# Optimization experiments

Hardware: AMD Instinct MI355X
Metric: run time of the kernel (lower is better)

The kernel has to match this reference:

```python
import jax, jax.numpy as jnp
import numpy as np

B, T, L, C = 64, 1024, 68, 2
H = 256  # hidden size per direction
D_IN = L * C  # 136


def setup_inputs() -> dict:
    key = jax.random.key(0)
    ks = jax.random.split(key, 8)
    s_ih = 0.05
    s_hh = 1.0 / np.sqrt(H)
    return {
        "x": jax.random.normal(ks[0], (B, T, L, C), dtype=jnp.float32),
        "w_ih_f": jax.random.normal(ks[1], (4 * H, D_IN), dtype=jnp.float32) * s_ih,
        "w_hh_f": jax.random.normal(ks[2], (4 * H, H), dtype=jnp.float32) * s_hh,
        "b_ih_f": jnp.zeros((4 * H,), jnp.float32),
        "b_hh_f": jnp.zeros((4 * H,), jnp.float32),
        "w_ih_b": jax.random.normal(ks[3], (4 * H, D_IN), dtype=jnp.float32) * s_ih,
        "w_hh_b": jax.random.normal(ks[4], (4 * H, H), dtype=jnp.float32) * s_hh,
        "b_ih_b": jnp.zeros((4 * H,), jnp.float32),
        "b_hh_b": jnp.zeros((4 * H,), jnp.float32),
        "fc_w": jax.random.normal(ks[5], (5, 2 * H), dtype=jnp.float32) * 0.06,
        "fc_b": jnp.zeros((5,), jnp.float32),
    }


def _lstm_scan(x_proj, w_hh, b_hh):
    """x_proj: (T, B, 4H) precomputed input projections. Returns hidden seq (T, B, H).
    PyTorch gate order: i, f, g, o."""
    h_dim = w_hh.shape[1]
    bsz = x_proj.shape[1]

    def step(carry, gx):
        h, c = carry
        g = gx + h @ w_hh.T + b_hh  # (B, 4H)
        i, f, gg, o = jnp.split(g, 4, axis=-1)
        i = jax.nn.sigmoid(i)
        f = jax.nn.sigmoid(f)
        gg = jnp.tanh(gg)
        o = jax.nn.sigmoid(o)
        c = f * c + i * gg
        h = o * jnp.tanh(c)
        return (h, c), h

    h0 = jnp.zeros((bsz, h_dim), x_proj.dtype)
    _, hs = jax.lax.scan(step, (h0, h0), x_proj)
    return hs


def reference(x, w_ih_f, w_hh_f, b_ih_f, b_hh_f, w_ih_b, w_hh_b, b_ih_b, b_hh_b, fc_w, fc_b):
    bsz, t = x.shape[0], x.shape[1]
    xf = x.reshape(bsz, t, -1)            # (B, T, 136)
    xt = jnp.transpose(xf, (1, 0, 2))     # (T, B, 136) time-major for scan
    # Precompute input-to-hidden projections for both directions (big GEMM, outside scan).
    proj_f = xt @ w_ih_f.T + b_ih_f       # (T, B, 4H)
    proj_b = xt[::-1] @ w_ih_b.T + b_ih_b # reversed time for backward direction
    hs_f = _lstm_scan(proj_f, w_hh_f, b_hh_f)           # (T, B, H)
    hs_b = _lstm_scan(proj_b, w_hh_b, b_hh_b)[::-1]     # flip back to forward time
    out = jnp.concatenate([hs_f, hs_b], axis=-1)        # (T, B, 2H)
    out = jnp.transpose(out, (1, 0, 2))                 # (B, T, 2H)
    # Dropout is identity in eval mode.
    return out @ fc_w.T + fc_b                          # (B, T, 5)
```

## Files before the change

kernel.cpp:

```cpp
#include <hip/hip_runtime.h>
#include <hip/hip_bf16.h>
#include <stdint.h>

#define B_    64
#define T_    1024
#define DIN   136
#define DINP  160
#define H_    256
#define G4H   1024

typedef __bf16 bf16;
typedef __bf16 bf16x8 __attribute__((ext_vector_type(8)));
typedef float  floatx4 __attribute__((ext_vector_type(4)));
typedef int    int4v  __attribute__((ext_vector_type(4)));

__global__ void k_pack_x(const float* __restrict__ x, bf16* __restrict__ xp) {
  const int n = T_ * B_ * DINP;
  for (int i = blockIdx.x * blockDim.x + threadIdx.x; i < n; i += gridDim.x * blockDim.x) {
    int k  = i % DINP;
    int tb = i / DINP;
    int b  = tb % B_;
    int t  = tb / B_;
    float v = 0.f;
    if (k < DIN) v = x[(b * T_ + t) * DIN + k];
    xp[i] = (bf16)v;
  }
}

__global__ void k_pack_whh(const float* __restrict__ wf, const float* __restrict__ wb,
                           bf16* __restrict__ wp) {
  const int n = 2 * G4H * H_;
  for (int i = blockIdx.x * blockDim.x + threadIdx.x; i < n; i += gridDim.x * blockDim.x) {
    int k   = i & (H_ - 1);
    int r   = (i >> 8) & (G4H - 1);
    int dir = i >> 18;
    int orig = ((r & 3) << 8) | (r >> 2);
    const float* w = dir ? wb : wf;
    wp[i] = (bf16)w[orig * H_ + k];
  }
}

__global__ void k_pack_wih(const float* __restrict__ wf, const float* __restrict__ wb,
                           bf16* __restrict__ wp) {
  const int n = 2 * G4H * DINP;
  for (int i = blockIdx.x * blockDim.x + threadIdx.x; i < n; i += gridDim.x * blockDim.x) {
    int k   = i % DINP;
    int r   = (i / DINP) & (G4H - 1);
    int dir = i / (G4H * DINP);
    int orig = ((r & 3) << 8) | (r >> 2);
    const float* w = dir ? wb : wf;
    float v = (k < DIN) ? w[orig * DIN + k] : 0.f;
    wp[i] = (bf16)v;
  }
}

__global__ void k_pack_bias(const float* __restrict__ bihf, const float* __restrict__ bhhf,
                            const float* __restrict__ bihb, const float* __restrict__ bhhb,
                            float* __restrict__ bs) {
  int i = blockIdx.x * blockDim.x + threadIdx.x;
  if (i >= 2 * G4H) return;
  int r = i & (G4H - 1); int dir = i >> 10;
  int orig = ((r & 3) << 8) | (r >> 2);
  bs[i] = dir ? (bihb[orig] + bhhb[orig]) : (bihf[orig] + bhhf[orig]);
}

__global__ __launch_bounds__(256, 1) void k_lstm(
    const bf16* __restrict__ xp, const bf16* __restrict__ whhp,
    const bf16* __restrict__ wihp, const float* __restrict__ bs,
    bf16* __restrict__ hbuf, unsigned* __restrict__ cnt)
{
  __shared__ bf16 h_sm[2 * 16 * 264];
  unsigned short* h_su = (unsigned short*)h_sm;

  const int tid = threadIdx.x;
  const int w   = tid >> 6;
  const int l   = tid & 63;
  const int q   = l >> 4;
  const int m   = l & 15;

  const int wgid  = blockIdx.x;
  const int g     = wgid >> 2;
  const int qtr   = wgid & 3;
  const int dir   = g >> 2;
  const int btile = g & 3;
  const int rowbase = qtr * 256 + w * 64;

  bf16x8 wf[4][8];
  bf16x8 wif[4][5];
  floatx4 bias[4];
#pragma unroll
  for (int tl = 0; tl < 4; ++tl) {
    const bf16* wr = whhp + (size_t)(dir * G4H + rowbase + tl * 16 + m) * H_ + q * 8;
#pragma unroll
    for (int s = 0; s < 8; ++s) {
      int kk = (qtr * 2 + s) & 7;
      wf[tl][s] = *(const bf16x8*)(wr + kk * 32);
    }
    const bf16* wr2 = wihp + (size_t)(dir * G4H + rowbase + tl * 16 + m) * DINP + q * 8;
#pragma unroll
    for (int kk = 0; kk < 5; ++kk) wif[tl][kk] = *(const bf16x8*)(wr2 + kk * 32);
    bias[tl] = *(const floatx4*)(bs + dir * G4H + rowbase + tl * 16 + q * 4);
  }

  unsigned* const cptr    = cnt + g * T_;
  unsigned* const hbuf_dw = (unsigned*)hbuf;
  const size_t hb_g = (size_t)g * T_;

  float cst[4] = {0.f, 0.f, 0.f, 0.f};

  bf16x8 xf[5];
  {
    const int xt0 = dir ? (T_ - 1) : 0;
    const bf16* xr = xp + (size_t)(xt0 * B_ + btile * 16 + m) * DINP + q * 8;
#pragma unroll
    for (int kk = 0; kk < 5; ++kk) xf[kk] = *(const bf16x8*)(xr + kk * 32);
  }

  for (int t = 0; t < T_; ++t) {
    const int xt = dir ? (T_ - 1 - t) : t;
    floatx4 acc[4] = {bias[0], bias[1], bias[2], bias[3]};

#pragma unroll
    for (int kk = 0; kk < 5; ++kk) {
#pragma unroll
      for (int tl = 0; tl < 4; ++tl)
        acc[tl] = __builtin_amdgcn_mfma_f32_16x16x32_bf16(wif[tl][kk], xf[kk], acc[tl], 0, 0, 0);
    }
    if (t + 1 < T_) {
      const int xtn = dir ? (T_ - 2 - t) : (t + 1);
      const bf16* xr = xp + (size_t)(xtn * B_ + btile * 16 + m) * DINP + q * 8;
#pragma unroll
      for (int kk = 0; kk < 5; ++kk) xf[kk] = *(const bf16x8*)(xr + kk * 32);
    }

    if (t > 0) {
      const int p = (t - 1) & 1;
      const bf16* hrow = &h_sm[(p * 16 + m) * 264 + q * 8];

#pragma unroll
      for (int s = 0; s < 2; ++s) {
        int kk = (qtr * 2 + s) & 7;
        bf16x8 bfr = *(const bf16x8*)(hrow + kk * 32);
#pragma unroll
        for (int tl = 0; tl < 4; ++tl)
          acc[tl] = __builtin_amdgcn_mfma_f32_16x16x32_bf16(wf[tl][s], bfr, acc[tl], 0, 0, 0);
      }

      {
        unsigned v;
        for (;;) {
          unsigned lv = 0;
          if (l == 0) lv = __hip_atomic_load(cptr + (t - 1), __ATOMIC_RELAXED, __HIP_MEMORY_SCOPE_AGENT);
          v = (unsigned)__shfl((int)lv, 0);
          if (v >= 16u) break;
          __builtin_amdgcn_s_sleep(1);
        }
      }
      __atomic_signal_fence(__ATOMIC_SEQ_CST);

      {
        const int xtp = dir ? (xt + 1) : (xt - 1);
        const size_t base_dw = (hb_g + xtp) * 16 * 128;
        const int mm = tid >> 4, jj = tid & 15;
        unsigned svals[6];
#pragma unroll
        for (int pp = 0; pp < 3; ++pp) {
          int qq = (qtr + 1 + pp) & 3;
          const unsigned* sp = hbuf_dw + base_dw + (size_t)mm * 128 + qq * 32 + jj;
          svals[pp * 2 + 0] = __hip_atomic_load(sp,      __ATOMIC_RELAXED, __HIP_MEMORY_SCOPE_AGENT);
          svals[pp * 2 + 1] = __hip_atomic_load(sp + 16, __ATOMIC_RELAXED, __HIP_MEMORY_SCOPE_AGENT);
        }
#pragma unroll
        for (int pp = 0; pp < 3; ++pp) {
          int qq = (qtr + 1 + pp) & 3;
          unsigned* dst = (unsigned*)&h_su[(p * 16 + mm) * 264 + qq * 64];
          dst[jj]      = svals[pp * 2 + 0];
          dst[jj + 16] = svals[pp * 2 + 1];
        }
      }
      __syncthreads();

#pragma unroll
      for (int s = 2; s < 8; ++s) {
        int kk = (qtr * 2 + s) & 7;
        bf16x8 bfr = *(const bf16x8*)(hrow + kk * 32);
#pragma unroll
        for (int tl = 0; tl < 4; ++tl)
          acc[tl] = __builtin_amdgcn_mfma_f32_16x16x32_bf16(wf[tl][s], bfr, acc[tl], 0, 0, 0);
      }
    }

    unsigned short hu[4];
#pragma unroll
    for (int tl = 0; tl < 4; ++tl) {
      float pi = acc[tl][0], pf = acc[tl][1], pg = acc[tl][2], po = acc[tl][3];
      float ig = 1.f / (1.f + __expf(-pi));
      float fg = 1.f / (1.f + __expf(-pf));
      float og = 1.f / (1.f + __expf(-po));
      float gcl = fminf(fmaxf(pg, -15.f), 15.f);
      float e2  = __expf(2.f * gcl);
      float gg  = (e2 - 1.f) / (e2 + 1.f);
      float c   = fg * cst[tl] + ig * gg;
      cst[tl]   = c;
      float ccl = fminf(fmaxf(c, -15.f), 15.f);
      float ec  = __expf(2.f * ccl);
      float hv  = og * ((ec - 1.f) / (ec + 1.f));
      bf16 hb = (bf16)hv;
      hu[tl] = __builtin_bit_cast(unsigned short, hb);
    }

    {
      const size_t obase = ((hb_g + xt) * 16 + m) * 128 + (size_t)(qtr * 32 + w * 8);
#pragma unroll
      for (int tl = 0; tl < 4; ++tl) {
        int ov = __shfl_xor((int)(unsigned)hu[tl], 16);
        if ((q & 1) == 0) {
          unsigned dw = (unsigned)hu[tl] | ((unsigned)ov << 16);
          __hip_atomic_store(hbuf_dw + obase + tl * 2 + (q >> 1), dw,
                             __ATOMIC_RELAXED, __HIP_MEMORY_SCOPE_AGENT);
        }
      }
    }

    {
      const int pcur = t & 1;
      const int hidl = qtr * 64 + w * 16 + q;
#pragma unroll
      for (int tl = 0; tl < 4; ++tl)
        h_su[(pcur * 16 + m) * 264 + hidl + tl * 4] = hu[tl];
    }

    asm volatile("s_waitcnt vmcnt(0)" ::: "memory");
    __atomic_signal_fence(__ATOMIC_SEQ_CST);
    if (l == 0)
      __hip_atomic_fetch_add(cptr + t, 1u, __ATOMIC_RELAXED, __HIP_MEMORY_SCOPE_AGENT);
    __syncthreads();
  }
}

__global__ __launch_bounds__(512) void k_fc(const bf16* __restrict__ hbuf,
                                            const float* __restrict__ fcw,
                                            const float* __restrict__ fcb,
                                            float* __restrict__ out)
{
  __shared__ float wsm[5 * 512];
  __shared__ unsigned short hl[64 * 258];
  const int tid = threadIdx.x;
  const int t   = blockIdx.x;
  for (int i = tid; i < 2560; i += 512) wsm[i] = fcw[i];
  const int o = tid / 64, b = tid & 63;
  float acc = 0.f;
  for (int dirc = 0; dirc < 2; ++dirc) {
    __syncthreads();
    for (int i = tid; i < 8192; i += 512) {
      int bb = i >> 7, dd = i & 127;
      int gg = dirc * 4 + (bb >> 4), mm = bb & 15;
      ((unsigned*)hl)[bb * 129 + dd] =
          ((const unsigned*)hbuf)[((size_t)(gg * T_ + t) * 16 + mm) * 128 + dd];
    }
    __syncthreads();
    if (tid < 320) {
      const float* wr = &wsm[o * 512 + dirc * 256];
      const unsigned short* hr = &hl[b * 258];
      float a = 0.f;
#pragma unroll 8
      for (int h = 0; h < 256; ++h) {
        unsigned u = ((unsigned)hr[h]) << 16;
        a += wr[h] * __builtin_bit_cast(float, u);
      }
      acc += a;
    }
  }
  if (tid < 320) out[((size_t)b * T_ + t) * 5 + o] = acc + fcb[o];
}

extern "C" void kernel_launch(void* const* d_in, const int* in_sizes, int n_in,
                              void* d_out, int out_size, void* d_ws, size_t ws_size,
                              hipStream_t stream) {
  const float* x    = (const float*)d_in[0];
  const float* wihf = (const float*)d_in[1];
  const float* whhf = (const float*)d_in[2];
  const float* bihf = (const float*)d_in[3];
  const float* bhhf = (const float*)d_in[4];
  const float* wihb = (const float*)d_in[5];
  const float* whhb = (const float*)d_in[6];
  const float* bihb = (const float*)d_in[7];
  const float* bhhb = (const float*)d_in[8];
  const float* fcw  = (const float*)d_in[9];
  const float* fcb  = (const float*)d_in[10];
  float* out = (float*)d_out;

  char* ws = (char*)d_ws;
  bf16*     xp   = (bf16*)(ws + 0);
  bf16*     whhp = (bf16*)(ws + 20971520);
  bf16*     wihp = (bf16*)(ws + 22020096);
  float*    bsum = (float*)(ws + 22675456);
  unsigned* cnt  = (unsigned*)(ws + 22683648);
  bf16*     hseq = (bf16*)(ws + 22716416);
  (void)in_sizes; (void)n_in; (void)out_size; (void)ws_size;

  hipMemsetAsync(cnt, 0, 8 * T_ * sizeof(unsigned), stream);
  k_pack_x   <<<4096, 256, 0, stream>>>(x, xp);
  k_pack_whh <<<1024, 256, 0, stream>>>(whhf, whhb, whhp);
  k_pack_wih <<<640,  256, 0, stream>>>(wihf, wihb, wihp);
  k_pack_bias<<<8,    256, 0, stream>>>(bihf, bhhf, bihb, bhhb, bsum);
  k_lstm     <<<32,   256, 0, stream>>>(xp, whhp, wihp, bsum, hseq, cnt);
  k_fc       <<<1024, 512, 0, stream>>>(hseq, fcw, fcb, out);
}
```

Before: 3.091 ms.

## Rewrite LSTM with int8 recurrent MFMA, single-block-per-group, segmented precomputed projections

Replaces the bf16 recurrent GEMM with int8 MFMA. Weights are quantized per tile, and h is split into hi and lo int8 parts to keep precision. Each batch tile now runs in one 1024-thread block, removing the cross-workgroup atomic flag sync. The input projection moves out of the recurrence into a separate fp16 GEMM kernel, run in four time segments that alternate with the LSTM and FC kernels, with state carried through global memory. Fast exp2/rcp activations are used. The extra kernel launches and the reduced-precision recurrence risk accuracy and add overhead.

```diff
diff --git a/kernel.cpp b/kernel.cpp
--- a/kernel.cpp
+++ b/kernel.cpp
@@ -8,36 +8,22 @@
 #define DINP  160
 #define H_    256
 #define G4H   1024
+#define SEG   256
+#define NSEG  4
 
 typedef __bf16 bf16;
+typedef _Float16 f16;
 typedef __bf16 bf16x8 __attribute__((ext_vector_type(8)));
 typedef float  floatx4 __attribute__((ext_vector_type(4)));
 typedef int    int4v  __attribute__((ext_vector_type(4)));
-
-__global__ void k_pack_x(const float* __restrict__ x, bf16* __restrict__ xp) {
-  const int n = T_ * B_ * DINP;
-  for (int i = blockIdx.x * blockDim.x + threadIdx.x; i < n; i += gridDim.x * blockDim.x) {
-    int k  = i % DINP;
-    int tb = i / DINP;
-    int b  = tb % B_;
-    int t  = tb / B_;
-    float v = 0.f;
-    if (k < DIN) v = x[(b * T_ + t) * DIN + k];
-    xp[i] = (bf16)v;
-  }
-}
-
-__global__ void k_pack_whh(const float* __restrict__ wf, const float* __restrict__ wb,
-                           bf16* __restrict__ wp) {
-  const int n = 2 * G4H * H_;
-  for (int i = blockIdx.x * blockDim.x + threadIdx.x; i < n; i += gridDim.x * blockDim.x) {
-    int k   = i & (H_ - 1);
-    int r   = (i >> 8) & (G4H - 1);
-    int dir = i >> 18;
-    int orig = ((r & 3) << 8) | (r >> 2);
-    const float* w = dir ? wb : wf;
-    wp[i] = (bf16)w[orig * H_ + k];
-  }
+typedef _Float16 half4 __attribute__((ext_vector_type(4)));
+
+__device__ __forceinline__ float fsigm(float x) {
+  return __builtin_amdgcn_rcpf(1.f + __builtin_amdgcn_exp2f(x * -1.4426950408889634f));
+}
+__device__ __forceinline__ float ftanh(float x) {
+  float e = __builtin_amdgcn_exp2f(x * 2.8853900817779268f);
+  return 1.f - 2.f * __builtin_amdgcn_rcpf(e + 1.f);
 }
 
 __global__ void k_pack_wih(const float* __restrict__ wf, const float* __restrict__ wb,
@@ -64,199 +50,244 @@
   bs[i] = dir ? (bihb[orig] + bhhb[orig]) : (bihf[orig] + bhhf[orig]);
 }
 
-__global__ __launch_bounds__(256, 1) void k_lstm(
-    const bf16* __restrict__ xp, const bf16* __restrict__ whhp,
-    const bf16* __restrict__ wihp, const float* __restrict__ bs,
-    bf16* __restrict__ hbuf, unsigned* __restrict__ cnt)
+__global__ __launch_bounds__(256) void k_pack_whh8(
+    const float* __restrict__ wf_, const float* __restrict__ wb_,
+    char* __restrict__ w8, float* __restrict__ scales)
 {
-  __shared__ bf16 h_sm[2 * 16 * 264];
-  unsigned short* h_su = (unsigned short*)h_sm;
-
+  __shared__ float red[4];
+  const int bx  = blockIdx.x;
+  const int dir = bx >> 6, Tt = bx & 63;
+  const float* w = dir ? wb_ : wf_;
   const int tid = threadIdx.x;
-  const int w   = tid >> 6;
-  const int l   = tid & 63;
-  const int q   = l >> 4;
-  const int m   = l & 15;
-
-  const int wgid  = blockIdx.x;
-  const int g     = wgid >> 2;
-  const int qtr   = wgid & 3;
-  const int dir   = g >> 2;
-  const int btile = g & 3;
-  const int rowbase = qtr * 256 + w * 64;
-
-  bf16x8 wf[4][8];
-  bf16x8 wif[4][5];
-  floatx4 bias[4];
+  const int c = tid >> 6, l = tid & 63, q = l >> 4, m = l & 15;
+  const int prow = Tt * 16 + m;
+  const int orig = ((prow & 3) << 8) | (prow >> 2);
+
+  float v[16]; float am = 0.f;
+#pragma unroll
+  for (int j = 0; j < 16; ++j) {
+    v[j] = w[orig * H_ + c * 64 + q * 16 + j];
+    am = fmaxf(am, fabsf(v[j]));
+  }
+#pragma unroll
+  for (int off = 32; off; off >>= 1) am = fmaxf(am, __shfl_xor(am, off));
+  if (l == 0) red[tid >> 6] = am;
+  __syncthreads();
+  am = fmaxf(fmaxf(red[0], red[1]), fmaxf(red[2], red[3]));
+  am = fmaxf(am, 1e-30f);
+  float qs = 127.f / am;
+
+  int4v o;
+#pragma unroll
+  for (int d = 0; d < 4; ++d) {
+    unsigned a8 = 0;
+#pragma unroll
+    for (int jj = 0; jj < 4; ++jj) {
+      int bi = (int)rintf(v[d * 4 + jj] * qs);
+      a8 |= ((unsigned)bi & 0xFFu) << (8 * jj);
+    }
+    o[d] = (int)a8;
+  }
+  ((int4v*)w8)[((size_t)(dir * 64 + Tt) * 4 + c) * 64 + l] = o;
+  if (tid == 0) scales[dir * 64 + Tt] = am / (127.f * 127.f * 256.f);
+}
+
+__global__ __launch_bounds__(256) void k_xproj(
+    const float* __restrict__ x, const bf16* __restrict__ wihp,
+    const float* __restrict__ bs, f16* __restrict__ xps, int seg)
+{
+  const int tid = threadIdx.x;
+  const int wv = tid >> 6, l = tid & 63, q = l >> 4, m = l & 15;
+  const int W = blockIdx.x * 4 + wv;
+  const int dir = W >> 10;
+  const int r = W & 1023;
+  const int j = r >> 2, b0 = (r & 3) * 16;
+  const int xt = dir ? (T_ - 1 - (seg * SEG + j)) : (seg * SEG + j);
+
+  bf16x8 a[5];
+  {
+    const float* xr = x + ((size_t)(b0 + m) * T_ + xt) * DIN;
+#pragma unroll
+    for (int c = 0; c < 5; ++c) {
+      bf16x8 av;
+#pragma unroll
+      for (int j8 = 0; j8 < 8; ++j8) {
+        int k = c * 32 + q * 8 + j8;
+        av[j8] = (k < DIN) ? (bf16)xr[k] : (bf16)0.f;
+      }
+      a[c] = av;
+    }
+  }
+
+  for (int nt = 0; nt < 64; ++nt) {
+    int col = nt * 16 + m;
+    float bv = bs[dir * G4H + col];
+    floatx4 acc = {bv, bv, bv, bv};
+    const bf16* wr = wihp + (size_t)(dir * G4H + col) * DINP + q * 8;
+#pragma unroll
+    for (int c = 0; c < 5; ++c)
+      acc = __builtin_amdgcn_mfma_f32_16x16x32_bf16(a[c], *(const bf16x8*)(wr + c * 32), acc, 0, 0, 0);
+#pragma unroll
+    for (int jj = 0; jj < 4; ++jj)
+      xps[((size_t)(dir * SEG + j) * B_ + b0 + q * 4 + jj) * G4H + col] = (f16)acc[jj];
+  }
+}
+
+__global__ __launch_bounds__(1024, 1) void k_lstm(
+    const int4v* __restrict__ whh8, const float* __restrict__ scales,
+    const f16* __restrict__ xps, bf16* __restrict__ hseg,
+    float* __restrict__ state, int seg)
+{
+  __shared__ char hsm[16384];
+
+  const int tid = threadIdx.x;
+  const int wv = tid >> 6, l = tid & 63, q = l >> 4, m = l & 15;
+  const int bx = blockIdx.x;
+  const int dir = bx >> 2, btile = bx & 3;
+
+  int4v wf[4][4];
+#pragma unroll
+  for (int tl = 0; tl < 4; ++tl)
+#pragma unroll
+    for (int c = 0; c < 4; ++c)
+      wf[tl][c] = whh8[((size_t)(dir * 64 + wv * 4 + tl) * 4 + c) * 64 + l];
+
+  float scl[4];
 #pragma unroll
   for (int tl = 0; tl < 4; ++tl) {
-    const bf16* wr = whhp + (size_t)(dir * G4H + rowbase + tl * 16 + m) * H_ + q * 8;
-#pragma unroll
-    for (int s = 0; s < 8; ++s) {
-      int kk = (qtr * 2 + s) & 7;
-      wf[tl][s] = *(const bf16x8*)(wr + kk * 32);
-    }
-    const bf16* wr2 = wihp + (size_t)(dir * G4H + rowbase + tl * 16 + m) * DINP + q * 8;
-#pragma unroll
-    for (int kk = 0; kk < 5; ++kk) wif[tl][kk] = *(const bf16x8*)(wr2 + kk * 32);
-    bias[tl] = *(const floatx4*)(bs + dir * G4H + rowbase + tl * 16 + q * 4);
-  }
-
-  unsigned* const cptr    = cnt + g * T_;
-  unsigned* const hbuf_dw = (unsigned*)hbuf;
-  const size_t hb_g = (size_t)g * T_;
+    float s = scales[dir * 64 + wv * 4 + tl];
+    scl[tl] = __builtin_bit_cast(float, __builtin_amdgcn_readfirstlane(__builtin_bit_cast(int, s)));
+  }
+
+  unsigned* const hseg_dw = (unsigned*)hseg;
+  const int cw = wv >> 2;
+  const int fl16 = (((wv & 3) * 16) + m) * 16;
 
   float cst[4] = {0.f, 0.f, 0.f, 0.f};
-
-  bf16x8 xf[5];
+  float hvf[4] = {0.f, 0.f, 0.f, 0.f};
+
+  if (seg > 0) {
+    const floatx4* sp = (const floatx4*)(state + ((size_t)bx * 1024 + tid) * 8);
+    floatx4 s0 = sp[0], s1 = sp[1];
+#pragma unroll
+    for (int tl = 0; tl < 4; ++tl) { cst[tl] = s0[tl]; hvf[tl] = s1[tl]; }
+#pragma unroll
+    for (int tl = 0; tl < 4; ++tl) {
+      float t127 = hvf[tl] * 127.f;
+      float fhi  = rintf(t127);
+      float flo  = fminf(fmaxf(rintf((t127 - fhi) * 256.f), -127.f), 127.f);
+      int waddr = ((1 * 2 + 0) * 4 + cw) * 1024 + fl16 + tl * 4 + q;
+      hsm[waddr]        = (char)(int)fhi;
+      hsm[waddr + 4096] = (char)(int)flo;
+    }
+  }
+
+  half4 nxt[4];
   {
-    const int xt0 = dir ? (T_ - 1) : 0;
-    const bf16* xr = xp + (size_t)(xt0 * B_ + btile * 16 + m) * DINP + q * 8;
-#pragma unroll
-    for (int kk = 0; kk < 5; ++kk) xf[kk] = *(const bf16x8*)(xr + kk * 32);
-  }
-
-  for (int t = 0; t < T_; ++t) {
-    const int xt = dir ? (T_ - 1 - t) : t;
-    floatx4 acc[4] = {bias[0], bias[1], bias[2], bias[3]};
-
-#pragma unroll
-    for (int kk = 0; kk < 5; ++kk) {
-#pragma unroll
-      for (int tl = 0; tl < 4; ++tl)
-        acc[tl] = __builtin_amdgcn_mfma_f32_16x16x32_bf16(wif[tl][kk], xf[kk], acc[tl], 0, 0, 0);
-    }
-    if (t + 1 < T_) {
-      const int xtn = dir ? (T_ - 2 - t) : (t + 1);
-      const bf16* xr = xp + (size_t)(xtn * B_ + btile * 16 + m) * DINP + q * 8;
-#pragma unroll
-      for (int kk = 0; kk < 5; ++kk) xf[kk] = *(const bf16x8*)(xr + kk * 32);
-    }
-
-    if (t > 0) {
-      const int p = (t - 1) & 1;
-      const bf16* hrow = &h_sm[(p * 16 + m) * 264 + q * 8];
-
-#pragma unroll
-      for (int s = 0; s < 2; ++s) {
-        int kk = (qtr * 2 + s) & 7;
-        bf16x8 bfr = *(const bf16x8*)(hrow + kk * 32);
+    const f16* ip = xps + ((size_t)(dir * SEG + 0) * B_ + btile * 16 + m) * G4H + wv * 64 + q * 4;
+#pragma unroll
+    for (int tl = 0; tl < 4; ++tl) nxt[tl] = *(const half4*)(ip + tl * 16);
+  }
+
+  for (int j = 0; j < SEG; ++j) {
+    const int tg = seg * SEG + j;
+    int4v a[4] = {{0,0,0,0},{0,0,0,0},{0,0,0,0},{0,0,0,0}};
+
+    if (tg > 0) {
+      __syncthreads();
+      const int pr = (tg & 1) ^ 1;
+#pragma unroll
+      for (int c = 0; c < 4; ++c) {
+        int4v bhi = *(const int4v*)(hsm + ((pr * 2 + 0) * 4 + c) * 1024 + l * 16);
 #pragma unroll
         for (int tl = 0; tl < 4; ++tl)
-          acc[tl] = __builtin_amdgcn_mfma_f32_16x16x32_bf16(wf[tl][s], bfr, acc[tl], 0, 0, 0);
-      }
-
-      {
-        unsigned v;
-        for (;;) {
-          unsigned lv = 0;
-          if (l == 0) lv = __hip_atomic_load(cptr + (t - 1), __ATOMIC_RELAXED, __HIP_MEMORY_SCOPE_AGENT);
-          v = (unsigned)__shfl((int)lv, 0);
-          if (v >= 16u) break;
-          __builtin_amdgcn_s_sleep(1);
-        }
-      }
-      __atomic_signal_fence(__ATOMIC_SEQ_CST);
-
-      {
-        const int xtp = dir ? (xt + 1) : (xt - 1);
-        const size_t base_dw = (hb_g + xtp) * 16 * 128;
-        const int mm = tid >> 4, jj = tid & 15;
-        unsigned svals[6];
-#pragma unroll
-        for (int pp = 0; pp < 3; ++pp) {
-          int qq = (qtr + 1 + pp) & 3;
-          const unsigned* sp = hbuf_dw + base_dw + (size_t)mm * 128 + qq * 32 + jj;
-          svals[pp * 2 + 0] = __hip_atomic_load(sp,      __ATOMIC_RELAXED, __HIP_MEMORY_SCOPE_AGENT);
-          svals[pp * 2 + 1] = __hip_atomic_load(sp + 16, __ATOMIC_RELAXED, __HIP_MEMORY_SCOPE_AGENT);
-        }
-#pragma unroll
-        for (int pp = 0; pp < 3; ++pp) {
-          int qq = (qtr + 1 + pp) & 3;
-          unsigned* dst = (unsigned*)&h_su[(p * 16 + mm) * 264 + qq * 64];
-          dst[jj]      = svals[pp * 2 + 0];
-          dst[jj + 16] = svals[pp * 2 + 1];
-        }
-      }
-      __syncthreads();
-
-#pragma unroll
-      for (int s = 2; s < 8; ++s) {
-        int kk = (qtr * 2 + s) & 7;
-        bf16x8 bfr = *(const bf16x8*)(hrow + kk * 32);
+          a[tl] = __builtin_amdgcn_mfma_i32_16x16x64_i8(wf[tl][c], bhi, a[tl], 0, 0, 0);
+      }
+#pragma unroll
+      for (int tl = 0; tl < 4; ++tl) a[tl] = a[tl] * 256;
+#pragma unroll
+      for (int c = 0; c < 4; ++c) {
+        int4v blo = *(const int4v*)(hsm + ((pr * 2 + 1) * 4 + c) * 1024 + l * 16);
 #pragma unroll
         for (int tl = 0; tl < 4; ++tl)
-          acc[tl] = __builtin_amdgcn_mfma_f32_16x16x32_bf16(wf[tl][s], bfr, acc[tl], 0, 0, 0);
+          a[tl] = __builtin_amdgcn_mfma_i32_16x16x64_i8(wf[tl][c], blo, a[tl], 0, 0, 0);
       }
     }
 
     unsigned short hu[4];
+    const int pw = tg & 1;
 #pragma unroll
     for (int tl = 0; tl < 4; ++tl) {
-      float pi = acc[tl][0], pf = acc[tl][1], pg = acc[tl][2], po = acc[tl][3];
-      float ig = 1.f / (1.f + __expf(-pi));
-      float fg = 1.f / (1.f + __expf(-pf));
-      float og = 1.f / (1.f + __expf(-po));
-      float gcl = fminf(fmaxf(pg, -15.f), 15.f);
-      float e2  = __expf(2.f * gcl);
-      float gg  = (e2 - 1.f) / (e2 + 1.f);
-      float c   = fg * cst[tl] + ig * gg;
-      cst[tl]   = c;
-      float ccl = fminf(fmaxf(c, -15.f), 15.f);
-      float ec  = __expf(2.f * ccl);
-      float hv  = og * ((ec - 1.f) / (ec + 1.f));
+      float s = scl[tl];
+      float pi = (float)nxt[tl][0] + (float)a[tl][0] * s;
+      float pf = (float)nxt[tl][1] + (float)a[tl][1] * s;
+      float pg = (float)nxt[tl][2] + (float)a[tl][2] * s;
+      float po = (float)nxt[tl][3] + (float)a[tl][3] * s;
+      float ig = fsigm(pi);
+      float fg = fsigm(pf);
+      float og = fsigm(po);
+      float gg = ftanh(pg);
+      float c  = fg * cst[tl] + ig * gg;
+      cst[tl]  = c;
+      float hv = og * ftanh(c);
+      hvf[tl]  = hv;
       bf16 hb = (bf16)hv;
       hu[tl] = __builtin_bit_cast(unsigned short, hb);
+
+      float t127 = hv * 127.f;
+      float fhi  = rintf(t127);
+      float flo  = fminf(fmaxf(rintf((t127 - fhi) * 256.f), -127.f), 127.f);
+      int waddr = ((pw * 2 + 0) * 4 + cw) * 1024 + fl16 + tl * 4 + q;
+      hsm[waddr]        = (char)(int)fhi;
+      hsm[waddr + 4096] = (char)(int)flo;
     }
 
     {
-      const size_t obase = ((hb_g + xt) * 16 + m) * 128 + (size_t)(qtr * 32 + w * 8);
+      const size_t obase = ((size_t)(bx * SEG + j) * 16 + m) * 128 + (size_t)(wv * 8);
 #pragma unroll
       for (int tl = 0; tl < 4; ++tl) {
         int ov = __shfl_xor((int)(unsigned)hu[tl], 16);
         if ((q & 1) == 0) {
           unsigned dw = (unsigned)hu[tl] | ((unsigned)ov << 16);
-          __hip_atomic_store(hbuf_dw + obase + tl * 2 + (q >> 1), dw,
-                             __ATOMIC_RELAXED, __HIP_MEMORY_SCOPE_AGENT);
+          hseg_dw[obase + tl * 2 + (q >> 1)] = dw;
         }
       }
     }
 
-    {
-      const int pcur = t & 1;
-      const int hidl = qtr * 64 + w * 16 + q;
-#pragma unroll
-      for (int tl = 0; tl < 4; ++tl)
-        h_su[(pcur * 16 + m) * 264 + hidl + tl * 4] = hu[tl];
-    }
-
-    asm volatile("s_waitcnt vmcnt(0)" ::: "memory");
-    __atomic_signal_fence(__ATOMIC_SEQ_CST);
-    if (l == 0)
-      __hip_atomic_fetch_add(cptr + t, 1u, __ATOMIC_RELAXED, __HIP_MEMORY_SCOPE_AGENT);
-    __syncthreads();
-  }
-}
-
-__global__ __launch_bounds__(512) void k_fc(const bf16* __restrict__ hbuf,
+    if (j + 1 < SEG) {
+      const f16* ip = xps + ((size_t)(dir * SEG + j + 1) * B_ + btile * 16 + m) * G4H + wv * 64 + q * 4;
+#pragma unroll
+      for (int tl = 0; tl < 4; ++tl) nxt[tl] = *(const half4*)(ip + tl * 16);
+    }
+  }
+
+  {
+    floatx4* sp = (floatx4*)(state + ((size_t)bx * 1024 + tid) * 8);
+    floatx4 s0, s1;
+#pragma unroll
+    for (int tl = 0; tl < 4; ++tl) { s0[tl] = cst[tl]; s1[tl] = hvf[tl]; }
+    sp[0] = s0; sp[1] = s1;
+  }
+}
+
+__global__ __launch_bounds__(512) void k_fc(const bf16* __restrict__ hseg,
                                             const float* __restrict__ fcw,
                                             const float* __restrict__ fcb,
-                                            float* __restrict__ out)
+                                            float* __restrict__ out, int seg)
 {
   __shared__ float wsm[5 * 512];
   __shared__ unsigned short hl[64 * 258];
   const int tid = threadIdx.x;
-  const int t   = blockIdx.x;
+  const int j   = blockIdx.x;
   for (int i = tid; i < 2560; i += 512) wsm[i] = fcw[i];
   const int o = tid / 64, b = tid & 63;
-  float acc = 0.f;
   for (int dirc = 0; dirc < 2; ++dirc) {
     __syncthreads();
     for (int i = tid; i < 8192; i += 512) {
       int bb = i >> 7, dd = i & 127;
-      int gg = dirc * 4 + (bb >> 4), mm = bb & 15;
+      int gg = dirc * 4 + (bb >> 4), mmx = bb & 15;
       ((unsigned*)hl)[bb * 129 + dd] =
-          ((const unsigned*)hbuf)[((size_t)(gg * T_ + t) * 16 + mm) * 128 + dd];
+          ((const unsigned*)hseg)[((size_t)(gg * SEG + j) * 16 + mmx) * 128 + dd];
     }
     __syncthreads();
     if (tid < 320) {
@@ -268,10 +299,11 @@
         unsigned u = ((unsigned)hr[h]) << 16;
         a += wr[h] * __builtin_bit_cast(float, u);
       }
-      acc += a;
-    }
-  }
-  if (tid < 320) out[((size_t)b * T_ + t) * 5 + o] = acc + fcb[o];
+      int tg = dirc ? (T_ - 1 - (seg * SEG + j)) : (seg * SEG + j);
+      size_t oi = ((size_t)b * T_ + tg) * 5 + o;
+      out[oi] += a + (dirc ? 0.f : fcb[o]);
+    }
+  }
 }
 
 extern "C" void kernel_launch(void* const* d_in, const int* in_sizes, int n_in,
@@ -291,19 +323,22 @@
   float* out = (float*)d_out;
 
   char* ws = (char*)d_ws;
-  bf16*     xp   = (bf16*)(ws + 0);
-  bf16*     whhp = (bf16*)(ws + 20971520);
-  bf16*     wihp = (bf16*)(ws + 22020096);
-  float*    bsum = (float*)(ws + 22675456);
-  unsigned* cnt  = (unsigned*)(ws + 22683648);
-  bf16*     hseq = (bf16*)(ws + 22716416);
-  (void)in_sizes; (void)n_in; (void)out_size; (void)ws_size;
-
-  hipMemsetAsync(cnt, 0, 8 * T_ * sizeof(unsigned), stream);
-  k_pack_x   <<<4096, 256, 0, stream>>>(x, xp);
-  k_pack_whh <<<1024, 256, 0, stream>>>(whhf, whhb, whhp);
-  k_pack_wih <<<640,  256, 0, stream>>>(wihf, wihb, wihp);
-  k_pack_bias<<<8,    256, 0, stream>>>(bihf, bhhf, bihb, bhhb, bsum);
-  k_lstm     <<<32,   256, 0, stream>>>(xp, whhp, wihp, bsum, hseq, cnt);
-  k_fc       <<<1024, 512, 0, stream>>>(hseq, fcw, fcb, out);
-}
+  bf16*  wihp  = (bf16*)(ws + 0);
+  float* bsum  = (float*)(ws + 655360);
+  int4v* whh8  = (int4v*)(ws + 663552);
+  float* scl   = (float*)(ws + 1187840);
+  f16*   xps   = (f16*)(ws + 1188352);
+  bf16*  hseg  = (bf16*)(ws + 68297216);
+  float* state = (float*)(ws + 85074432);
+  (void)in_sizes; (void)n_in; (void)ws_size;
+
+  hipMemsetAsync(out, 0, (size_t)out_size * sizeof(float), stream);
+  k_pack_wih <<<640, 256, 0, stream>>>(wihf, wihb, wihp);
+  k_pack_bias<<<8,   256, 0, stream>>>(bihf, bhhf, bihb, bhhb, bsum);
+  k_pack_whh8<<<128, 256, 0, stream>>>(whhf, whhb, (char*)whh8, scl);
+  for (int s = 0; s < NSEG; ++s) {
+    k_xproj<<<512, 256, 0, stream>>>(x, wihp, bsum, xps, s);
+    k_lstm <<<8,  1024, 0, stream>>>(whh8, scl, xps, hseg, state, s);
+    k_fc   <<<256, 512, 0, stream>>>(hseg, fcw, fcb, out, s);
+  }
+}
```

After: 3.976 ms. 1.29x slower.
